# Kernel optimization log

Hardware: AMD Instinct MI355X
Metric: run time of the kernel (lower is better)

Reference implementation:

```python
import jax, jax.numpy as jnp
import numpy as np
from jax import lax

D_L, D_A, D_V = 300, 74, 35
Z = 256   # zl/za/zv size (LSTM hidden)
F = 128   # fl/fa/fv size
OUT = 1
T, N = 64, 4096


def _p(key, shape, scale=0.05):
    return (jax.random.normal(key, shape, dtype=jnp.float32) * scale)


def setup_inputs() -> dict:
    key = jax.random.key(0)
    ks = iter(jax.random.split(key, 64))
    inp = {"x": jax.random.normal(next(ks), (T, N, D_L + D_A + D_V), dtype=jnp.float32)}
    for m, d in (("l", D_L), ("a", D_A), ("v", D_V)):
        inp[f"W_ih_{m}"] = _p(next(ks), (4 * Z, d))
        inp[f"W_hh_{m}"] = _p(next(ks), (4 * Z, Z))
        inp[f"b_ih_{m}"] = _p(next(ks), (4 * Z,))
        inp[f"b_hh_{m}"] = _p(next(ks), (4 * Z,))
        inp[f"Wfc_{m}"] = _p(next(ks), (Z, Z))
        inp[f"bfc_{m}"] = _p(next(ks), (Z,))
        inp[f"Wh1_{m}"] = _p(next(ks), (F, Z))
        inp[f"bh1_{m}"] = _p(next(ks), (F,))
        inp[f"Wh2_{m}"] = _p(next(ks), (F, F))
        inp[f"bh2_{m}"] = _p(next(ks), (F,))
    inp["Wy"] = _p(next(ks), (OUT, 3 * F))
    inp["by"] = _p(next(ks), (OUT,))
    return inp


def _lstm_encode(x_seq, W_ih, W_hh, b_ih, b_hh, Wfc, bfc):
    # x_seq: [t, n, d]; PyTorch LSTMCell gate order: i, f, g, o
    n = x_seq.shape[1]
    h = x_seq.dtype
    gates_x = jnp.einsum('tnd,gd->tng', x_seq, W_ih) + b_ih + b_hh  # [t,n,4Z]

    def step(carry, gx):
        hx, cx = carry
        gates = gx + hx @ W_hh.T
        i, f, g, o = jnp.split(gates, 4, axis=1)
        i = jax.nn.sigmoid(i); f = jax.nn.sigmoid(f)
        g = jnp.tanh(g);       o = jax.nn.sigmoid(o)
        cx = f * cx + i * g
        hx = o * jnp.tanh(cx)
        return (hx, cx), None

    init = (jnp.zeros((n, Z), dtype=h), jnp.zeros((n, Z), dtype=h))
    (last_h, _), _ = lax.scan(step, init, gates_x)
    return last_h @ Wfc.T + bfc  # encoderLSTM.fc1


def _head(z, W1, b1, W2, b2):
    # relu(fc2(dropout(relu(fc1(z))))) with dropout p=0 (eval)
    return jax.nn.relu(jax.nn.relu(z @ W1.T + b1) @ W2.T + b2)


def reference(x,
              W_ih_l, W_hh_l, b_ih_l, b_hh_l, Wfc_l, bfc_l, Wh1_l, bh1_l, Wh2_l, bh2_l,
              W_ih_a, W_hh_a, b_ih_a, b_hh_a, Wfc_a, bfc_a, Wh1_a, bh1_a, Wh2_a, bh2_a,
              W_ih_v, W_hh_v, b_ih_v, b_hh_v, Wfc_v, bfc_v, Wh1_v, bh1_v, Wh2_v, bh2_v,
              Wy, by):
    x_l = x[:, :, :D_L]
    x_a = x[:, :, D_L:D_L + D_A]
    x_v = x[:, :, D_L + D_A:]
    zl = _lstm_encode(x_l, W_ih_l, W_hh_l, b_ih_l, b_hh_l, Wfc_l, bfc_l)
    za = _lstm_encode(x_a, W_ih_a, W_hh_a, b_ih_a, b_hh_a, Wfc_a, bfc_a)
    zv = _lstm_encode(x_v, W_ih_v, W_hh_v, b_ih_v, b_hh_v, Wfc_v, bfc_v)
    fl = _head(zl, Wh1_l, bh1_l, Wh2_l, bh2_l)
    fa = _head(za, Wh1_a, bh1_a, Wh2_a, bh2_a)
    fv = _head(zv, Wh1_v, bh1_v, Wh2_v, bh2_v)
    fs = jnp.concatenate([fl, fa, fv], axis=1)
    y_hat = fs @ Wy.T + by
    # original returns ([x_l, x_a, x_v, y_hat], mmd_loss=0.0, missing_loss=0.0)
    return x_l, x_a, x_v, y_hat


if __name__ == "__main__":
    out = reference(**setup_inputs())
    print([o.shape for o in out])
```

## Files before the change

### kernel.cpp

```cpp
#include <hip/hip_runtime.h>

typedef __attribute__((ext_vector_type(8))) short short8;
typedef __attribute__((ext_vector_type(4))) float f32x4;
typedef unsigned short ushort_t;

#define T_DIM 64
#define N_DIM 4096
#define DL 300
#define DA 74
#define DV 35
#define DTOT 409
#define ZD 256
#define FD 128
#define KP1_L 320
#define KP1_A 96
#define KP1_V 64
#define KC_L ((KP1_L + 256) / 32)
#define KC_A ((KP1_A + 256) / 32)
#define KC_V ((KP1_V + 256) / 32)

__device__ __forceinline__ ushort_t f2bf(float v) {
    unsigned u = __float_as_uint(v);
    u += 0x7fffu + ((u >> 16) & 1u);
    return (ushort_t)(u >> 16);
}

__device__ __forceinline__ float fastrcp(float x) {
#if __has_builtin(__builtin_amdgcn_rcpf)
    return __builtin_amdgcn_rcpf(x);
#else
    return 1.f / x;
#endif
}

__device__ __forceinline__ void async_lds16(const ushort_t* g, ushort_t* l) {
    __builtin_amdgcn_global_load_lds(
        (const __attribute__((address_space(1))) unsigned int*)g,
        (__attribute__((address_space(3))) unsigned int*)l, 16, 0, 0);
}

struct PrepP {
    const float* x;
    float* ol;
    float* oa;
    float* ov;
    ushort_t* xf[3];
};
__global__ __launch_bounds__(256) void prep_kernel(PrepP p) {
    __shared__ float xrow[16][420];
    const int bid = blockIdx.x;
    const int t = bid >> 8, nb = bid & 255;
    const int tid = threadIdx.x;
    const size_t rowbase = (size_t)t * N_DIM + (size_t)nb * 16;

    const float* __restrict__ src = p.x + rowbase * DTOT;
    for (int e = tid; e < 16 * DTOT; e += 256) {
        int r = e / DTOT, d = e - r * DTOT;
        xrow[r][d] = src[e];
    }
    __syncthreads();

    {
        float* __restrict__ dl = p.ol + rowbase * DL;
        for (int e = tid; e < 16 * DL; e += 256) { int r = e / DL, d = e - r * DL; dl[e] = xrow[r][d]; }
        float* __restrict__ da = p.oa + rowbase * DA;
        for (int e = tid; e < 16 * DA; e += 256) { int r = e / DA, d = e - r * DA; da[e] = xrow[r][300 + d]; }
        float* __restrict__ dv = p.ov + rowbase * DV;
        for (int e = tid; e < 16 * DV; e += 256) { int r = e / DV, d = e - r * DV; dv[e] = xrow[r][374 + d]; }
    }

    const unsigned tnb = (unsigned)t * 256u + (unsigned)nb;
    for (int q = tid; q < 960; q += 256) {
        int m, kc, l, xkc, col0, dcap;
        if (q < 640)      { m = 0; kc = q >> 6;          l = q & 63; xkc = 10; col0 = 0;   dcap = DL; }
        else if (q < 832) { int qq = q - 640; m = 1; kc = qq >> 6; l = qq & 63; xkc = 3; col0 = 300; dcap = DA; }
        else              { int qq = q - 832; m = 2; kc = qq >> 6; l = qq & 63; xkc = 2; col0 = 374; dcap = DV; }
        int n16 = l & 15;
        int kb = kc * 32 + (l >> 4) * 8;
        ushort_t tmp[8];
#pragma unroll
        for (int j = 0; j < 8; ++j) {
            int k = kb + j;
            tmp[j] = (k < dcap) ? f2bf(xrow[n16][col0 + k]) : (ushort_t)0;
        }
        ushort_t* dst = p.xf[m] + (((size_t)tnb * xkc + kc) * 64 + l) * 8;
        *reinterpret_cast<short8*>(dst) = *reinterpret_cast<short8*>(tmp);
    }
}

struct WConvP {
    const float* Wih[3];
    const float* Whh[3];
    ushort_t* wf[3];
};
__global__ __launch_bounds__(256) void wconv_kernel(WConvP p) {
    const unsigned CL = 16u * 4 * KC_L * 64;
    const unsigned CA = 16u * 4 * KC_A * 64;
    const unsigned CV = 16u * 4 * KC_V * 64;
    unsigned e = blockIdx.x * 256u + threadIdx.x;
    int m, kcm, d, kp1;
    unsigned rel;
    if (e < CL)                { m = 0; rel = e;           kcm = KC_L; d = DL; kp1 = KP1_L; }
    else if (e < CL + CA)      { m = 1; rel = e - CL;      kcm = KC_A; d = DA; kp1 = KP1_A; }
    else if (e < CL + CA + CV) { m = 2; rel = e - CL - CA; kcm = KC_V; d = DV; kp1 = KP1_V; }
    else return;
    unsigned lane = rel & 63u;
    unsigned rest = rel >> 6;
    unsigned kc = rest % (unsigned)kcm;
    unsigned zg = rest / (unsigned)kcm;
    unsigned g = zg & 3u, zs = zg >> 2;
    unsigned row = g * 256u + zs * 16u + (lane & 15u);
    unsigned kb = kc * 32u + (lane >> 4) * 8u;
    const float* __restrict__ Wih = p.Wih[m];
    const float* __restrict__ Whh = p.Whh[m];
    ushort_t tmp[8];
#pragma unroll
    for (int j = 0; j < 8; ++j) {
        int k = (int)kb + j;
        float v = 0.f;
        if (k < d) v = Wih[(size_t)row * d + k];
        else if (k >= kp1) v = Whh[(size_t)row * 256u + (k - kp1)];
        tmp[j] = f2bf(v);
    }
    *reinterpret_cast<short8*>(p.wf[m] + (size_t)rel * 8) = *reinterpret_cast<short8*>(tmp);
}

struct ChainP {
    const ushort_t* xf[3];
    const ushort_t* wf[3];
    const float* bih[3];
    const float* bhh[3];
    float* hf;
};

template <int KP1>
__device__ __forceinline__ void chain_body(const ChainP& p, int m, int row0, ushort_t* sh) {
    constexpr int XKC = KP1 / 32;
    constexpr int KC = XKC + 8;
    constexpr int XCH = 4 * XKC;
    constexpr int XSZ = XCH * 512;
    const int tid = threadIdx.x;
    const int w = tid >> 6, lane = tid & 63, ln = lane & 15, lg = lane >> 4;
    const int nb0 = row0 >> 4;

    ushort_t* hb0 = sh;
    ushort_t* xb0 = sh + 32768;
    const ushort_t* __restrict__ xf = p.xf[m];
    const ushort_t* __restrict__ wf = p.wf[m];

    for (int e = tid; e < 8192; e += 512) ((unsigned*)hb0)[e] = 0u;

    for (int q = w; q < XCH; q += 8) {
        int rf = q / XKC, kc = q - rf * XKC;
        const ushort_t* src = xf + (((size_t)0 * 256 + nb0 + rf) * XKC + kc) * 512 + lane * 8;
        async_lds16(src, xb0 + (size_t)q * 512);
    }

    float bb4[2][4];
#pragma unroll
    for (int pp = 0; pp < 2; ++pp) {
        int z = pp * 128 + w * 16 + ln;
        bb4[pp][0] = p.bih[m][z] + p.bhh[m][z];
        bb4[pp][1] = p.bih[m][256 + z] + p.bhh[m][256 + z];
        bb4[pp][2] = p.bih[m][512 + z] + p.bhh[m][512 + z];
        bb4[pp][3] = p.bih[m][768 + z] + p.bhh[m][768 + z];
    }
    float creg[2][4][4] = {};
    asm volatile("s_waitcnt vmcnt(0)" ::: "memory");
    __syncthreads();

#pragma unroll 1
    for (int t = 0; t < T_DIM; ++t) {
        const ushort_t* __restrict__ xbc = xb0 + (size_t)(t & 1) * XSZ;
        const ushort_t* __restrict__ hbc = hb0 + (size_t)(t & 1) * 16384;
        ushort_t* __restrict__ hbn = hb0 + (size_t)((t & 1) ^ 1) * 16384;

        if (t + 1 < T_DIM) {
            ushort_t* xbn = xb0 + (size_t)((t & 1) ^ 1) * XSZ;
            for (int q = w; q < XCH; q += 8) {
                int rf = q / XKC, kc = q - rf * XKC;
                const ushort_t* src =
                    xf + (((size_t)(t + 1) * 256 + nb0 + rf) * XKC + kc) * 512 + lane * 8;
                async_lds16(src, xbn + (size_t)q * 512);
            }
        }

#pragma unroll
        for (int pp = 0; pp < 2; ++pp) {
            const int zs = pp * 8 + w;
            const ushort_t* __restrict__ wfz = wf + (size_t)zs * 4 * KC * 512;
            f32x4 acc[4][4] = {};
            short8 bcur[4];
#pragma unroll
            for (int g = 0; g < 4; ++g)
                bcur[g] = *reinterpret_cast<const short8*>(
                    wfz + ((size_t)g * KC) * 512 + lane * 8);
#pragma unroll 1
            for (int kc = 0; kc < KC; ++kc) {
                short8 bnxt[4];
                if (kc + 1 < KC) {
#pragma unroll
                    for (int g = 0; g < 4; ++g)
                        bnxt[g] = *reinterpret_cast<const short8*>(
                            wfz + ((size_t)g * KC + kc + 1) * 512 + lane * 8);
                }
                short8 a[4];
                if (kc < XKC) {
#pragma unroll
                    for (int rf = 0; rf < 4; ++rf)
                        a[rf] = *reinterpret_cast<const short8*>(
                            xbc + ((size_t)(rf * XKC + kc) * 64 + lane) * 8);
                } else {
#pragma unroll
                    for (int rf = 0; rf < 4; ++rf)
                        a[rf] = *reinterpret_cast<const short8*>(
                            hbc + ((size_t)(rf * 8 + (kc - XKC)) * 64 + lane) * 8);
                }
#pragma unroll
                for (int g = 0; g < 4; ++g)
#pragma unroll
                    for (int rf = 0; rf < 4; ++rf)
                        acc[rf][g] = __builtin_amdgcn_mfma_f32_16x16x32_bf16(
                            a[rf], bcur[g], acc[rf][g], 0, 0, 0);
                if (kc + 1 < KC) {
#pragma unroll
                    for (int g = 0; g < 4; ++g) bcur[g] = bnxt[g];
                }
            }
            const int z = pp * 128 + w * 16 + ln;
            const int kc2 = z >> 5;
            const int bofs = ((z >> 3) & 3) * 16;
            const int jj = z & 7;
#pragma unroll
            for (int rf = 0; rf < 4; ++rf) {
#pragma unroll
                for (int reg = 0; reg < 4; ++reg) {
                    float gi = acc[rf][0][reg] + bb4[pp][0];
                    float gf = acc[rf][1][reg] + bb4[pp][1];
                    float gg = acc[rf][2][reg] + bb4[pp][2];
                    float go = acc[rf][3][reg] + bb4[pp][3];
                    float i_ = fastrcp(1.f + __expf(-gi));
                    float f_ = fastrcp(1.f + __expf(-gf));
                    float g_ = 1.f - 2.f * fastrcp(1.f + __expf(2.f * gg));
                    float o_ = fastrcp(1.f + __expf(-go));
                    float cc = f_ * creg[pp][rf][reg] + i_ * g_;
                    creg[pp][rf][reg] = cc;
                    float hh = o_ * (1.f - 2.f * fastrcp(1.f + __expf(2.f * cc)));
                    hbn[((size_t)(rf * 8 + kc2) * 64 + (lg * 4 + reg + bofs)) * 8 + jj] = f2bf(hh);
                    if (t == T_DIM - 1) {
                        int nl = rf * 16 + lg * 4 + reg;
                        p.hf[(size_t)m * N_DIM * ZD + (size_t)(row0 + nl) * ZD + z] = hh;
                    }
                }
            }
        }

        asm volatile("s_waitcnt vmcnt(0)" ::: "memory");
        __syncthreads();
    }
}

__global__ __launch_bounds__(512, 1) void lstm_chain_kernel(ChainP p) {
    __shared__ ushort_t sh[73728];
    const int bid = blockIdx.x;
    const int r8 = bid & 7, idx = bid >> 3;
    const int m = idx >> 3;
    const int bm = (idx & 7) * 8 + r8;
    const int row0 = bm * 64;
    if (m == 0)      chain_body<KP1_L>(p, 0, row0, sh);
    else if (m == 1) chain_body<KP1_A>(p, 1, row0, sh);
    else             chain_body<KP1_V>(p, 2, row0, sh);
}

struct GemmP {
    const float* A1[3];
    const float* W1[3];
    const float* b1[3];
    float* C[3];
    int K1[3];
    int lda1;
    int ldc;
    int relu;
};

__device__ __forceinline__ void mac16(const float (&As)[16][64], const float (&Ws)[16][64],
                                      int tx, int ty, float (&acc)[4][4]) {
#pragma unroll
    for (int k = 0; k < 16; ++k) {
        float4 av = *reinterpret_cast<const float4*>(&As[k][ty * 4]);
        float4 bv = *reinterpret_cast<const float4*>(&Ws[k][tx * 4]);
        float a[4] = {av.x, av.y, av.z, av.w};
        float b[4] = {bv.x, bv.y, bv.z, bv.w};
#pragma unroll
        for (int i = 0; i < 4; ++i)
#pragma unroll
            for (int j = 0; j < 4; ++j)
                acc[i][j] = fmaf(a[i], b[j], acc[i][j]);
    }
}

__global__ __launch_bounds__(256) void gemm3_kernel(GemmP p) {
    const int m = blockIdx.z;
    const float* __restrict__ A1 = p.A1[m];
    const float* __restrict__ W1 = p.W1[m];
    const int K1 = p.K1[m];
    float* __restrict__ C = p.C[m];
    const int row0 = blockIdx.x * 64;
    const int col0 = blockIdx.y * 64;

    __shared__ __align__(16) float As[16][64];
    __shared__ __align__(16) float Ws[16][64];

    const int tid = threadIdx.x;
    const int tx = tid & 15, ty = tid >> 4;
    float acc[4][4] = {};

    for (int k0 = 0; k0 < K1; k0 += 16) {
#pragma unroll
        for (int i = 0; i < 4; ++i) {
            int e = tid * 4 + i;
            int rr = e >> 4, k = e & 15;
            int kk = k0 + k;
            As[k][rr] = (kk < K1) ? A1[(size_t)(row0 + rr) * p.lda1 + kk] : 0.f;
            Ws[k][rr] = (kk < K1) ? W1[(size_t)(col0 + rr) * K1 + kk] : 0.f;
        }
        __syncthreads();
        mac16(As, Ws, tx, ty, acc);
        __syncthreads();
    }

    const float* __restrict__ b1 = p.b1[m];
#pragma unroll
    for (int i = 0; i < 4; ++i) {
        int rr = row0 + ty * 4 + i;
        float v[4];
#pragma unroll
        for (int j = 0; j < 4; ++j) {
            int cc = col0 + tx * 4 + j;
            float tvl = acc[i][j] + b1[cc];
            if (p.relu) tvl = fmaxf(tvl, 0.f);
            v[j] = tvl;
        }
        float4 o = make_float4(v[0], v[1], v[2], v[3]);
        *reinterpret_cast<float4*>(&C[(size_t)rr * p.ldc + col0 + tx * 4]) = o;
    }
}

__global__ __launch_bounds__(256) void y_kernel(const float* __restrict__ fs,
                                                const float* __restrict__ Wy,
                                                const float* __restrict__ by,
                                                float* __restrict__ y) {
    unsigned wave = (blockIdx.x * 256u + threadIdx.x) >> 6;
    unsigned lane = threadIdx.x & 63u;
    if (wave >= N_DIM) return;
    const float* row = fs + (size_t)wave * 3 * FD;
    float s = 0.f;
    for (unsigned j = lane; j < 3 * FD; j += 64) s += row[j] * Wy[j];
#pragma unroll
    for (int off = 32; off; off >>= 1) s += __shfl_down(s, off);
    if (lane == 0) y[wave] = s + by[0];
}

extern "C" void kernel_launch(void* const* d_in, const int* in_sizes, int n_in,
                              void* d_out, int out_size, void* d_ws, size_t ws_size,
                              hipStream_t stream) {
    const float* x = (const float*)d_in[0];
    const float *W_ih[3], *W_hh[3], *b_ih[3], *b_hh[3], *Wfc[3], *bfc[3],
                *Wh1[3], *bh1[3], *Wh2[3], *bh2[3];
    for (int m = 0; m < 3; ++m) {
        const int b = 1 + m * 10;
        W_ih[m] = (const float*)d_in[b + 0];
        W_hh[m] = (const float*)d_in[b + 1];
        b_ih[m] = (const float*)d_in[b + 2];
        b_hh[m] = (const float*)d_in[b + 3];
        Wfc[m]  = (const float*)d_in[b + 4];
        bfc[m]  = (const float*)d_in[b + 5];
        Wh1[m]  = (const float*)d_in[b + 6];
        bh1[m]  = (const float*)d_in[b + 7];
        Wh2[m]  = (const float*)d_in[b + 8];
        bh2[m]  = (const float*)d_in[b + 9];
    }
    const float* Wy = (const float*)d_in[31];
    const float* by = (const float*)d_in[32];

    float* out   = (float*)d_out;
    float* out_l = out;
    float* out_a = out_l + (size_t)T_DIM * N_DIM * DL;
    float* out_v = out_a + (size_t)T_DIM * N_DIM * DA;
    float* out_y = out_v + (size_t)T_DIM * N_DIM * DV;

    const size_t NZ = (size_t)N_DIM * ZD;
    const size_t NF = (size_t)N_DIM * FD;
    const size_t WFL = (size_t)16 * 4 * KC_L * 512;
    const size_t WFA = (size_t)16 * 4 * KC_A * 512;
    const size_t WFV = (size_t)16 * 4 * KC_V * 512;

    char* wsb = (char*)d_ws;
    float* hf   = (float*)wsb;
    float* zbuf = hf + 3 * NZ;
    float* f1   = zbuf + 3 * NZ;
    float* fs   = f1 + 3 * NF;
    ushort_t* wf_l = (ushort_t*)(fs + 3 * NF);
    ushort_t* wf_a = wf_l + WFL;
    ushort_t* wf_v = wf_a + WFA;
    ushort_t* xf_l = wf_v + WFV;
    ushort_t* xf_a = xf_l + (size_t)T_DIM * N_DIM * KP1_L;
    ushort_t* xf_v = xf_a + (size_t)T_DIM * N_DIM * KP1_A;
    size_t need = (size_t)((char*)(xf_v + (size_t)T_DIM * N_DIM * KP1_V) - wsb);
    if (ws_size < need) return;

    {
        WConvP p{};
        for (int m = 0; m < 3; ++m) { p.Wih[m] = W_ih[m]; p.Whh[m] = W_hh[m]; }
        p.wf[0] = wf_l; p.wf[1] = wf_a; p.wf[2] = wf_v;
        wconv_kernel<<<(16 * 4 * (KC_L + KC_A + KC_V) * 64) / 256, 256, 0, stream>>>(p);
    }

    {
        PrepP p{};
        p.x = x;
        p.ol = out_l; p.oa = out_a; p.ov = out_v;
        p.xf[0] = xf_l; p.xf[1] = xf_a; p.xf[2] = xf_v;
        prep_kernel<<<T_DIM * 256, 256, 0, stream>>>(p);
    }

    {
        ChainP cp{};
        cp.xf[0] = xf_l; cp.xf[1] = xf_a; cp.xf[2] = xf_v;
        cp.wf[0] = wf_l; cp.wf[1] = wf_a; cp.wf[2] = wf_v;
        for (int m = 0; m < 3; ++m) { cp.bih[m] = b_ih[m]; cp.bhh[m] = b_hh[m]; }
        cp.hf = hf;
        lstm_chain_kernel<<<192, 512, 0, stream>>>(cp);
    }

    {
        GemmP p{};
        for (int m = 0; m < 3; ++m) {
            p.A1[m] = hf + m * NZ; p.W1[m] = Wfc[m]; p.K1[m] = ZD;
            p.b1[m] = bfc[m];      p.C[m] = zbuf + m * NZ;
        }
        p.lda1 = ZD; p.ldc = ZD; p.relu = 0;
        gemm3_kernel<<<dim3(N_DIM / 64, ZD / 64, 3), 256, 0, stream>>>(p);
    }
    {
        GemmP p{};
        for (int m = 0; m < 3; ++m) {
            p.A1[m] = zbuf + m * NZ; p.W1[m] = Wh1[m]; p.K1[m] = ZD;
            p.b1[m] = bh1[m];        p.C[m] = f1 + m * NF;
        }
        p.lda1 = ZD; p.ldc = FD; p.relu = 1;
        gemm3_kernel<<<dim3(N_DIM / 64, FD / 64, 3), 256, 0, stream>>>(p);
    }
    {
        GemmP p{};
        for (int m = 0; m < 3; ++m) {
            p.A1[m] = f1 + m * NF; p.W1[m] = Wh2[m]; p.K1[m] = FD;
            p.b1[m] = bh2[m];      p.C[m] = fs + m * FD;
        }
        p.lda1 = FD; p.ldc = 3 * FD; p.relu = 1;
        gemm3_kernel<<<dim3(N_DIM / 64, FD / 64, 3), 256, 0, stream>>>(p);
    }
    y_kernel<<<(N_DIM * 64) / 256, 256, 0, stream>>>(fs, Wy, by, out_y);
}
```

Baseline: 1.460 ms.

## Rebalance LSTM chain blocks: split language modality across more blocks, deepen weight prefetch

The language-modality LSTM, which has the largest input width, now runs with 32 rows per block instead of 64, so the grid grows from 192 to 256 blocks on the 256-CU MI355X and the critical-path block does less work. The weight B-fragment loads move from a one-deep register double-buffer to a 3–4 deep rotating prefetch, and the K loop is fully unrolled. The next-timestep x prefetch is issued after the first gate-group GEMM rather than at the start of the step. The trade-offs are higher register pressure and twice as many weight reads per language row.

```diff
diff --git a/kernel.cpp b/kernel.cpp
--- a/kernel.cpp
+++ b/kernel.cpp
@@ -133,22 +133,24 @@
     float* hf;
 };
 
-template <int KP1>
+template <int KP1, int RF>
 __device__ __forceinline__ void chain_body(const ChainP& p, int m, int row0, ushort_t* sh) {
     constexpr int XKC = KP1 / 32;
     constexpr int KC = XKC + 8;
-    constexpr int XCH = 4 * XKC;
+    constexpr int XCH = RF * XKC;
     constexpr int XSZ = XCH * 512;
+    constexpr int HSZ = RF * 4096;
+    constexpr int PF = (RF == 2) ? 4 : 3;
     const int tid = threadIdx.x;
     const int w = tid >> 6, lane = tid & 63, ln = lane & 15, lg = lane >> 4;
     const int nb0 = row0 >> 4;
 
     ushort_t* hb0 = sh;
-    ushort_t* xb0 = sh + 32768;
+    ushort_t* xb0 = sh + 2 * HSZ;
     const ushort_t* __restrict__ xf = p.xf[m];
     const ushort_t* __restrict__ wf = p.wf[m];
 
-    for (int e = tid; e < 8192; e += 512) ((unsigned*)hb0)[e] = 0u;
+    for (int e = tid; e < RF * 2048; e += 512) ((unsigned*)hb0)[e] = 0u;
 
     for (int q = w; q < XCH; q += 8) {
         int rf = q / XKC, kc = q - rf * XKC;
@@ -165,74 +167,73 @@
         bb4[pp][2] = p.bih[m][512 + z] + p.bhh[m][512 + z];
         bb4[pp][3] = p.bih[m][768 + z] + p.bhh[m][768 + z];
     }
-    float creg[2][4][4] = {};
+    float creg[2][RF][4] = {};
     asm volatile("s_waitcnt vmcnt(0)" ::: "memory");
     __syncthreads();
 
 #pragma unroll 1
     for (int t = 0; t < T_DIM; ++t) {
         const ushort_t* __restrict__ xbc = xb0 + (size_t)(t & 1) * XSZ;
-        const ushort_t* __restrict__ hbc = hb0 + (size_t)(t & 1) * 16384;
-        ushort_t* __restrict__ hbn = hb0 + (size_t)((t & 1) ^ 1) * 16384;
-
-        if (t + 1 < T_DIM) {
-            ushort_t* xbn = xb0 + (size_t)((t & 1) ^ 1) * XSZ;
-            for (int q = w; q < XCH; q += 8) {
-                int rf = q / XKC, kc = q - rf * XKC;
-                const ushort_t* src =
-                    xf + (((size_t)(t + 1) * 256 + nb0 + rf) * XKC + kc) * 512 + lane * 8;
-                async_lds16(src, xbn + (size_t)q * 512);
-            }
-        }
+        const ushort_t* __restrict__ hbc = hb0 + (size_t)(t & 1) * HSZ;
+        ushort_t* __restrict__ hbn = hb0 + (size_t)((t & 1) ^ 1) * HSZ;
 
 #pragma unroll
         for (int pp = 0; pp < 2; ++pp) {
             const int zs = pp * 8 + w;
             const ushort_t* __restrict__ wfz = wf + (size_t)zs * 4 * KC * 512;
-            f32x4 acc[4][4] = {};
-            short8 bcur[4];
-#pragma unroll
-            for (int g = 0; g < 4; ++g)
-                bcur[g] = *reinterpret_cast<const short8*>(
-                    wfz + ((size_t)g * KC) * 512 + lane * 8);
-#pragma unroll 1
+            f32x4 acc[RF][4] = {};
+            short8 bbuf[PF][4];
+#pragma unroll
+            for (int i = 0; i < PF; ++i)
+#pragma unroll
+                for (int g = 0; g < 4; ++g)
+                    bbuf[i][g] = *reinterpret_cast<const short8*>(
+                        wfz + ((size_t)g * KC + i) * 512 + lane * 8);
+
+#pragma unroll
             for (int kc = 0; kc < KC; ++kc) {
-                short8 bnxt[4];
-                if (kc + 1 < KC) {
-#pragma unroll
-                    for (int g = 0; g < 4; ++g)
-                        bnxt[g] = *reinterpret_cast<const short8*>(
-                            wfz + ((size_t)g * KC + kc + 1) * 512 + lane * 8);
-                }
-                short8 a[4];
+                short8 a[RF];
                 if (kc < XKC) {
 #pragma unroll
-                    for (int rf = 0; rf < 4; ++rf)
+                    for (int rf = 0; rf < RF; ++rf)
                         a[rf] = *reinterpret_cast<const short8*>(
                             xbc + ((size_t)(rf * XKC + kc) * 64 + lane) * 8);
                 } else {
 #pragma unroll
-                    for (int rf = 0; rf < 4; ++rf)
+                    for (int rf = 0; rf < RF; ++rf)
                         a[rf] = *reinterpret_cast<const short8*>(
                             hbc + ((size_t)(rf * 8 + (kc - XKC)) * 64 + lane) * 8);
                 }
 #pragma unroll
                 for (int g = 0; g < 4; ++g)
 #pragma unroll
-                    for (int rf = 0; rf < 4; ++rf)
+                    for (int rf = 0; rf < RF; ++rf)
                         acc[rf][g] = __builtin_amdgcn_mfma_f32_16x16x32_bf16(
-                            a[rf], bcur[g], acc[rf][g], 0, 0, 0);
-                if (kc + 1 < KC) {
-#pragma unroll
-                    for (int g = 0; g < 4; ++g) bcur[g] = bnxt[g];
+                            a[rf], bbuf[kc % PF][g], acc[rf][g], 0, 0, 0);
+                if (kc + PF < KC) {
+#pragma unroll
+                    for (int g = 0; g < 4; ++g)
+                        bbuf[kc % PF][g] = *reinterpret_cast<const short8*>(
+                            wfz + ((size_t)g * KC + kc + PF) * 512 + lane * 8);
                 }
             }
+
+            if (pp == 0 && t + 1 < T_DIM) {
+                ushort_t* xbn = xb0 + (size_t)((t & 1) ^ 1) * XSZ;
+                for (int q = w; q < XCH; q += 8) {
+                    int rf = q / XKC, kc = q - rf * XKC;
+                    const ushort_t* src =
+                        xf + (((size_t)(t + 1) * 256 + nb0 + rf) * XKC + kc) * 512 + lane * 8;
+                    async_lds16(src, xbn + (size_t)q * 512);
+                }
+            }
+
             const int z = pp * 128 + w * 16 + ln;
             const int kc2 = z >> 5;
             const int bofs = ((z >> 3) & 3) * 16;
             const int jj = z & 7;
 #pragma unroll
-            for (int rf = 0; rf < 4; ++rf) {
+            for (int rf = 0; rf < RF; ++rf) {
 #pragma unroll
                 for (int reg = 0; reg < 4; ++reg) {
                     float gi = acc[rf][0][reg] + bb4[pp][0];
@@ -261,15 +262,19 @@
 }
 
 __global__ __launch_bounds__(512, 1) void lstm_chain_kernel(ChainP p) {
-    __shared__ ushort_t sh[73728];
+    __shared__ ushort_t sh[45056];
     const int bid = blockIdx.x;
     const int r8 = bid & 7, idx = bid >> 3;
-    const int m = idx >> 3;
-    const int bm = (idx & 7) * 8 + r8;
-    const int row0 = bm * 64;
-    if (m == 0)      chain_body<KP1_L>(p, 0, row0, sh);
-    else if (m == 1) chain_body<KP1_A>(p, 1, row0, sh);
-    else             chain_body<KP1_V>(p, 2, row0, sh);
+    if (idx < 16) {
+        const int bm = idx * 8 + r8;
+        chain_body<KP1_L, 2>(p, 0, bm * 32, sh);
+    } else if (idx < 24) {
+        const int bm = (idx - 16) * 8 + r8;
+        chain_body<KP1_A, 4>(p, 1, bm * 64, sh);
+    } else {
+        const int bm = (idx - 24) * 8 + r8;
+        chain_body<KP1_V, 4>(p, 2, bm * 64, sh);
+    }
 }
 
 struct GemmP {
@@ -430,7 +435,7 @@
         cp.wf[0] = wf_l; cp.wf[1] = wf_a; cp.wf[2] = wf_v;
         for (int m = 0; m < 3; ++m) { cp.bih[m] = b_ih[m]; cp.bhh[m] = b_hh[m]; }
         cp.hf = hf;
-        lstm_chain_kernel<<<192, 512, 0, stream>>>(cp);
+        lstm_chain_kernel<<<256, 512, 0, stream>>>(cp);
     }
 
     {
```

Result: slower. 3.010 ms (+106.1%).

## Use 16 waves per LSTM block, one z-slice per wave, prefetch x after MFMA

Applied to the files above, without the earlier changes.

The recurrent chain kernel now launches 1024 threads, 16 waves per block. Each wave owns one 16-column z-slice instead of looping over two, halving serial per-wave work per timestep and raising MFMA parallelism within a CU. The async prefetch of the next timestep's x tile is moved after the MFMA loop, and the hidden-buffer zeroing and prefetch strides are adjusted for the wider block. The register budget per thread drops under the 1024-thread launch bound, which risks spills, and more waves now contend for the same LDS.

```diff
diff --git a/kernel.cpp b/kernel.cpp
--- a/kernel.cpp
+++ b/kernel.cpp
@@ -140,7 +140,8 @@
     constexpr int XCH = 4 * XKC;
     constexpr int XSZ = XCH * 512;
     const int tid = threadIdx.x;
-    const int w = tid >> 6, lane = tid & 63, ln = lane & 15, lg = lane >> 4;
+    const int w = tid >> 6;
+    const int lane = tid & 63, ln = lane & 15, lg = lane >> 4;
     const int nb0 = row0 >> 4;
 
     ushort_t* hb0 = sh;
@@ -148,26 +149,27 @@
     const ushort_t* __restrict__ xf = p.xf[m];
     const ushort_t* __restrict__ wf = p.wf[m];
 
-    for (int e = tid; e < 8192; e += 512) ((unsigned*)hb0)[e] = 0u;
-
-    for (int q = w; q < XCH; q += 8) {
+    for (int e = tid; e < 8192; e += 1024) ((unsigned*)hb0)[e] = 0u;
+
+    for (int q = w; q < XCH; q += 16) {
         int rf = q / XKC, kc = q - rf * XKC;
         const ushort_t* src = xf + (((size_t)0 * 256 + nb0 + rf) * XKC + kc) * 512 + lane * 8;
         async_lds16(src, xb0 + (size_t)q * 512);
     }
 
-    float bb4[2][4];
-#pragma unroll
-    for (int pp = 0; pp < 2; ++pp) {
-        int z = pp * 128 + w * 16 + ln;
-        bb4[pp][0] = p.bih[m][z] + p.bhh[m][z];
-        bb4[pp][1] = p.bih[m][256 + z] + p.bhh[m][256 + z];
-        bb4[pp][2] = p.bih[m][512 + z] + p.bhh[m][512 + z];
-        bb4[pp][3] = p.bih[m][768 + z] + p.bhh[m][768 + z];
-    }
-    float creg[2][4][4] = {};
+    const int z = w * 16 + ln;
+    float bb4[4];
+#pragma unroll
+    for (int g = 0; g < 4; ++g)
+        bb4[g] = p.bih[m][g * 256 + z] + p.bhh[m][g * 256 + z];
+    float creg[4][4] = {};
     asm volatile("s_waitcnt vmcnt(0)" ::: "memory");
     __syncthreads();
+
+    const int kc2 = z >> 5;
+    const int bofs = ((z >> 3) & 3) * 16;
+    const int jj = z & 7;
+    const ushort_t* __restrict__ wfz = wf + (size_t)w * 4 * KC * 512;
 
 #pragma unroll 1
     for (int t = 0; t < T_DIM; ++t) {
@@ -175,9 +177,48 @@
         const ushort_t* __restrict__ hbc = hb0 + (size_t)(t & 1) * 16384;
         ushort_t* __restrict__ hbn = hb0 + (size_t)((t & 1) ^ 1) * 16384;
 
+        f32x4 acc[4][4] = {};
+        short8 bcur[4];
+#pragma unroll
+        for (int g = 0; g < 4; ++g)
+            bcur[g] = *reinterpret_cast<const short8*>(
+                wfz + ((size_t)g * KC) * 512 + lane * 8);
+#pragma unroll 1
+        for (int kc = 0; kc < KC; ++kc) {
+            short8 bnxt[4];
+            if (kc + 1 < KC) {
+#pragma unroll
+                for (int g = 0; g < 4; ++g)
+                    bnxt[g] = *reinterpret_cast<const short8*>(
+                        wfz + ((size_t)g * KC + kc + 1) * 512 + lane * 8);
+            }
+            short8 a[4];
+            if (kc < XKC) {
+#pragma unroll
+                for (int rf = 0; rf < 4; ++rf)
+                    a[rf] = *reinterpret_cast<const short8*>(
+                        xbc + ((size_t)(rf * XKC + kc) * 64 + lane) * 8);
+            } else {
+#pragma unroll
+                for (int rf = 0; rf < 4; ++rf)
+                    a[rf] = *reinterpret_cast<const short8*>(
+                        hbc + ((size_t)(rf * 8 + (kc - XKC)) * 64 + lane) * 8);
+            }
+#pragma unroll
+            for (int g = 0; g < 4; ++g)
+#pragma unroll
+                for (int rf = 0; rf < 4; ++rf)
+                    acc[rf][g] = __builtin_amdgcn_mfma_f32_16x16x32_bf16(
+                        a[rf], bcur[g], acc[rf][g], 0, 0, 0);
+            if (kc + 1 < KC) {
+#pragma unroll
+                for (int g = 0; g < 4; ++g) bcur[g] = bnxt[g];
+            }
+        }
+
         if (t + 1 < T_DIM) {
             ushort_t* xbn = xb0 + (size_t)((t & 1) ^ 1) * XSZ;
-            for (int q = w; q < XCH; q += 8) {
+            for (int q = w; q < XCH; q += 16) {
                 int rf = q / XKC, kc = q - rf * XKC;
                 const ushort_t* src =
                     xf + (((size_t)(t + 1) * 256 + nb0 + rf) * XKC + kc) * 512 + lane * 8;
@@ -186,73 +227,26 @@
         }
 
 #pragma unroll
-        for (int pp = 0; pp < 2; ++pp) {
-            const int zs = pp * 8 + w;
-            const ushort_t* __restrict__ wfz = wf + (size_t)zs * 4 * KC * 512;
-            f32x4 acc[4][4] = {};
-            short8 bcur[4];
-#pragma unroll
-            for (int g = 0; g < 4; ++g)
-                bcur[g] = *reinterpret_cast<const short8*>(
-                    wfz + ((size_t)g * KC) * 512 + lane * 8);
-#pragma unroll 1
-            for (int kc = 0; kc < KC; ++kc) {
-                short8 bnxt[4];
-                if (kc + 1 < KC) {
-#pragma unroll
-                    for (int g = 0; g < 4; ++g)
-                        bnxt[g] = *reinterpret_cast<const short8*>(
-                            wfz + ((size_t)g * KC + kc + 1) * 512 + lane * 8);
-                }
-                short8 a[4];
-                if (kc < XKC) {
-#pragma unroll
-                    for (int rf = 0; rf < 4; ++rf)
-                        a[rf] = *reinterpret_cast<const short8*>(
-                            xbc + ((size_t)(rf * XKC + kc) * 64 + lane) * 8);
-                } else {
-#pragma unroll
-                    for (int rf = 0; rf < 4; ++rf)
-                        a[rf] = *reinterpret_cast<const short8*>(
-                            hbc + ((size_t)(rf * 8 + (kc - XKC)) * 64 + lane) * 8);
-                }
-#pragma unroll
-                for (int g = 0; g < 4; ++g)
-#pragma unroll
-                    for (int rf = 0; rf < 4; ++rf)
-                        acc[rf][g] = __builtin_amdgcn_mfma_f32_16x16x32_bf16(
-                            a[rf], bcur[g], acc[rf][g], 0, 0, 0);
-                if (kc + 1 < KC) {
-#pragma unroll
-                    for (int g = 0; g < 4; ++g) bcur[g] = bnxt[g];
+        for (int rf = 0; rf < 4; ++rf) {
+#pragma unroll
+            for (int reg = 0; reg < 4; ++reg) {
+                float gi = acc[rf][0][reg] + bb4[0];
+                float gf = acc[rf][1][reg] + bb4[1];
+                float gg = acc[rf][2][reg] + bb4[2];
+                float go = acc[rf][3][reg] + bb4[3];
+                float i_ = fastrcp(1.f + __expf(-gi));
+                float f_ = fastrcp(1.f + __expf(-gf));
+                float g_ = 1.f - 2.f * fastrcp(1.f + __expf(2.f * gg));
+                float o_ = fastrcp(1.f + __expf(-go));
+                float cc = f_ * creg[rf][reg] + i_ * g_;
+                creg[rf][reg] = cc;
+                float hh = o_ * (1.f - 2.f * fastrcp(1.f + __expf(2.f * cc)));
+                hbn[((size_t)(rf * 8 + kc2) * 64 + (lg * 4 + reg + bofs)) * 8 + jj] = f2bf(hh);
+                if (t == T_DIM - 1) {
+                    int nl = rf * 16 + lg * 4 + reg;
+                    p.hf[(size_t)m * N_DIM * ZD + (size_t)(row0 + nl) * ZD + z] = hh;
                 }
             }
-            const int z = pp * 128 + w * 16 + ln;
-            const int kc2 = z >> 5;
-            const int bofs = ((z >> 3) & 3) * 16;
-            const int jj = z & 7;
-#pragma unroll
-            for (int rf = 0; rf < 4; ++rf) {
-#pragma unroll
-                for (int reg = 0; reg < 4; ++reg) {
-                    float gi = acc[rf][0][reg] + bb4[pp][0];
-                    float gf = acc[rf][1][reg] + bb4[pp][1];
-                    float gg = acc[rf][2][reg] + bb4[pp][2];
-                    float go = acc[rf][3][reg] + bb4[pp][3];
-                    float i_ = fastrcp(1.f + __expf(-gi));
-                    float f_ = fastrcp(1.f + __expf(-gf));
-                    float g_ = 1.f - 2.f * fastrcp(1.f + __expf(2.f * gg));
-                    float o_ = fastrcp(1.f + __expf(-go));
-                    float cc = f_ * creg[pp][rf][reg] + i_ * g_;
-                    creg[pp][rf][reg] = cc;
-                    float hh = o_ * (1.f - 2.f * fastrcp(1.f + __expf(2.f * cc)));
-                    hbn[((size_t)(rf * 8 + kc2) * 64 + (lg * 4 + reg + bofs)) * 8 + jj] = f2bf(hh);
-                    if (t == T_DIM - 1) {
-                        int nl = rf * 16 + lg * 4 + reg;
-                        p.hf[(size_t)m * N_DIM * ZD + (size_t)(row0 + nl) * ZD + z] = hh;
-                    }
-                }
-            }
         }
 
         asm volatile("s_waitcnt vmcnt(0)" ::: "memory");
@@ -260,7 +254,7 @@
     }
 }
 
-__global__ __launch_bounds__(512, 1) void lstm_chain_kernel(ChainP p) {
+__global__ __launch_bounds__(1024, 1) void lstm_chain_kernel(ChainP p) {
     __shared__ ushort_t sh[73728];
     const int bid = blockIdx.x;
     const int r8 = bid & 7, idx = bid >> 3;
@@ -430,7 +424,7 @@
         cp.wf[0] = wf_l; cp.wf[1] = wf_a; cp.wf[2] = wf_v;
         for (int m = 0; m < 3; ++m) { cp.bih[m] = b_ih[m]; cp.bhh[m] = b_hh[m]; }
         cp.hf = hf;
-        lstm_chain_kernel<<<192, 512, 0, stream>>>(cp);
+        lstm_chain_kernel<<<192, 1024, 0, stream>>>(cp);
     }
 
     {
```

After: 1.660 ms. 1.14x slower.
